# Kernel optimization log

Hardware: AMD Instinct MI355X
Metric: run time of the kernel (lower is better)

The kernel has to match this reference:

```python
import jax, jax.numpy as jnp
import numpy as np

N_NODES = 100000
N_EDGES = 300000
D_NODE_IN = 128
D_EDGE_IN = 4
LATENT = 256
HIDDEN = 256
STEPS = 6
D_OUT = 128
LN_EPS = 1e-5


def _mlp(x, w1, b1, w2, b2):
    # hk.nets.MLP([HIDDEN, out], activation=swish): act on hidden, none on output
    return jax.nn.swish(x @ w1 + b1) @ w2 + b2


def _ln(x, scale, offset):
    m = jnp.mean(x, axis=-1, keepdims=True)
    c = x - m
    v = jnp.mean(c * c, axis=-1, keepdims=True)
    return c * jax.lax.rsqrt(v + LN_EPS) * scale + offset


def setup_inputs():
    key = jax.random.key(0)
    ks = iter(jax.random.split(key, 40))

    def w(shape):
        fan_in = shape[-2]
        return (jax.random.normal(next(ks), shape, jnp.float32) / np.sqrt(fan_in).astype(np.float32))

    inp = {}
    inp['node_features'] = jax.random.normal(next(ks), (N_NODES, D_NODE_IN), jnp.float32)
    inp['edge_features'] = jax.random.normal(next(ks), (N_EDGES, D_EDGE_IN), jnp.float32)
    inp['senders'] = jax.random.randint(next(ks), (N_EDGES,), 0, N_NODES, jnp.int32)
    inp['receivers'] = jax.random.randint(next(ks), (N_EDGES,), 0, N_NODES, jnp.int32)
    # encoder (embed) MLPs + LayerNorm
    inp['enc_node_w1'] = w((D_NODE_IN, HIDDEN)); inp['enc_node_b1'] = jnp.zeros((HIDDEN,), jnp.float32)
    inp['enc_node_w2'] = w((HIDDEN, LATENT)); inp['enc_node_b2'] = jnp.zeros((LATENT,), jnp.float32)
    inp['enc_node_ln_s'] = jnp.ones((LATENT,), jnp.float32); inp['enc_node_ln_o'] = jnp.zeros((LATENT,), jnp.float32)
    inp['enc_edge_w1'] = w((D_EDGE_IN, HIDDEN)); inp['enc_edge_b1'] = jnp.zeros((HIDDEN,), jnp.float32)
    inp['enc_edge_w2'] = w((HIDDEN, LATENT)); inp['enc_edge_b2'] = jnp.zeros((LATENT,), jnp.float32)
    inp['enc_edge_ln_s'] = jnp.ones((LATENT,), jnp.float32); inp['enc_edge_ln_o'] = jnp.zeros((LATENT,), jnp.float32)
    # processor: STEPS unshared InteractionNetwork layers, weights stacked on axis 0
    inp['pe_w1'] = w((STEPS, 3 * LATENT, HIDDEN)); inp['pe_b1'] = jnp.zeros((STEPS, HIDDEN), jnp.float32)
    inp['pe_w2'] = w((STEPS, HIDDEN, LATENT)); inp['pe_b2'] = jnp.zeros((STEPS, LATENT), jnp.float32)
    inp['pe_ln_s'] = jnp.ones((STEPS, LATENT), jnp.float32); inp['pe_ln_o'] = jnp.zeros((STEPS, LATENT), jnp.float32)
    inp['pn_w1'] = w((STEPS, 2 * LATENT, HIDDEN)); inp['pn_b1'] = jnp.zeros((STEPS, HIDDEN), jnp.float32)
    inp['pn_w2'] = w((STEPS, HIDDEN, LATENT)); inp['pn_b2'] = jnp.zeros((STEPS, LATENT), jnp.float32)
    inp['pn_ln_s'] = jnp.ones((STEPS, LATENT), jnp.float32); inp['pn_ln_o'] = jnp.zeros((STEPS, LATENT), jnp.float32)
    # decoder (output) MLP, no LayerNorm
    inp['dec_w1'] = w((LATENT, HIDDEN)); inp['dec_b1'] = jnp.zeros((HIDDEN,), jnp.float32)
    inp['dec_w2'] = w((HIDDEN, D_OUT)); inp['dec_b2'] = jnp.zeros((D_OUT,), jnp.float32)
    return inp


def reference(node_features, edge_features, senders, receivers,
              enc_node_w1, enc_node_b1, enc_node_w2, enc_node_b2, enc_node_ln_s, enc_node_ln_o,
              enc_edge_w1, enc_edge_b1, enc_edge_w2, enc_edge_b2, enc_edge_ln_s, enc_edge_ln_o,
              pe_w1, pe_b1, pe_w2, pe_b2, pe_ln_s, pe_ln_o,
              pn_w1, pn_b1, pn_w2, pn_b2, pn_ln_s, pn_ln_o,
              dec_w1, dec_b1, dec_w2, dec_b2):
    # Embed nodes and edges into latent space (MLP + LayerNorm).
    node = _ln(_mlp(node_features, enc_node_w1, enc_node_b1, enc_node_w2, enc_node_b2), enc_node_ln_s, enc_node_ln_o)
    edge = _ln(_mlp(edge_features, enc_edge_w1, enc_edge_b1, enc_edge_w2, enc_edge_b2), enc_edge_ln_s, enc_edge_ln_o)

    n_nodes = node.shape[0]

    def step(carry, p):
        node, edge = carry
        ew1, eb1, ew2, eb2, els, elo, nw1, nb1, nw2, nb2, nls, nlo = p
        # edge update: MLP(concat[edge, sender_node, receiver_node]) + residual
        msg_in = jnp.concatenate([edge, node[senders], node[receivers]], axis=-1)  # [E, 3*LATENT]
        edge = edge + _ln(_mlp(msg_in, ew1, eb1, ew2, eb2), els, elo)
        # aggregate messages to receiver nodes
        agg = jax.ops.segment_sum(edge, receivers, num_segments=n_nodes)  # [N, LATENT]
        # node update: MLP(concat[node, agg]) + residual
        node = node + _ln(_mlp(jnp.concatenate([node, agg], axis=-1), nw1, nb1, nw2, nb2), nls, nlo)
        return (node, edge), None

    (node, edge), _ = jax.lax.scan(
        step, (node, edge),
        (pe_w1, pe_b1, pe_w2, pe_b2, pe_ln_s, pe_ln_o,
         pn_w1, pn_b1, pn_w2, pn_b2, pn_ln_s, pn_ln_o))

    # decoder: plain MLP (no LayerNorm) on nodes only (node_output_size given).
    return _mlp(node, dec_w1, dec_b1, dec_w2, dec_b2)  # [N, D_OUT]
```

## Files before the change

kernel.cpp:

```cpp
#include <hip/hip_runtime.h>
#include <hip/hip_bf16.h>


#define NN 100000
#define NE 300000

typedef __attribute__((ext_vector_type(8))) short bf16x8;
typedef __attribute__((ext_vector_type(8))) unsigned short u16x8;
typedef __attribute__((ext_vector_type(4))) float f32x4;

typedef const __attribute__((address_space(1))) void cg1_t;
typedef __attribute__((address_space(3))) void l3_t;
static __device__ __forceinline__ void gld_lds16(const void* g, void* l) {
  __builtin_amdgcn_global_load_lds((cg1_t*)g, (l3_t*)l, 16, 0, 0);
}

static __device__ __forceinline__ unsigned short f2bf(float f) {
  union { float f; unsigned u; } v; v.f = f;
  unsigned r = v.u + 0x7FFFu + ((v.u >> 16) & 1u);
  return (unsigned short)(r >> 16);
}
static __device__ __forceinline__ float bf2f(unsigned short h) {
  union { unsigned u; float f; } v; v.u = ((unsigned)h) << 16;
  return v.f;
}
static __device__ __forceinline__ float swish(float x) {
  return x * __builtin_amdgcn_rcpf(1.f + __expf(-x));
}

struct KArgs {
  const float* Xf;
  unsigned short* nodeB;
  unsigned short* edgeB;
  const unsigned short* aggB;
  const int* snd;
  const int* rcv;
  const unsigned short* W1p;
  const unsigned short* W2p;
  const float* b1;
  const float* b2;
  const float* lns;
  const float* lno;
  float* outF;
  int M;
};

__global__ void pack_w(const float* __restrict__ src,
                       unsigned short* __restrict__ dst,
                       int Ksrc, int Kpad, int N) {
  src += (size_t)blockIdx.y * Ksrc * N;
  dst += (size_t)blockIdx.y * Kpad * N;
  int fi = blockIdx.x;
  int nfr = N >> 4;
  int nb = fi % nfr, kb = fi / nfr;
  int t = threadIdx.x;
  int lane = t >> 3, j = t & 7;
  int k = kb * 32 + ((lane >> 4) * 8) + j;
  int col = nb * 16 + (lane & 15);
  unsigned short v = (k < Ksrc) ? f2bf(src[(size_t)k * N + col]) : (unsigned short)0;
  dst[(size_t)fi * 512 + t] = v;
}

__global__ void zero_ws(uint4* __restrict__ p, int n16) {
  uint4 z = {0u, 0u, 0u, 0u};
  for (int i = blockIdx.x * blockDim.x + threadIdx.x; i < n16;
       i += gridDim.x * blockDim.x)
    p[i] = z;
}

__global__ void hist_k(const int* __restrict__ rcv, int* __restrict__ cnt) {
  int e = blockIdx.x * blockDim.x + threadIdx.x;
  if (e < NE) {
    int r = rcv[e]; r = r < 0 ? 0 : (r > NN - 1 ? NN - 1 : r);
    atomicAdd(&cnt[r], 1);
  }
}

__global__ __launch_bounds__(1024)
void scan_k(const int* __restrict__ cnt, int* __restrict__ off) {
  __shared__ int wsum[16];
  __shared__ int carry_s, tot_s;
  int t = threadIdx.x, lane = t & 63, w = t >> 6;
  if (t == 0) carry_s = 0;
  __syncthreads();
  for (int base = 0; base < NN; base += 1024) {
    int i = base + t;
    int v = (i < NN) ? cnt[i] : 0;
    int incl = v;
    #pragma unroll
    for (int d = 1; d < 64; d <<= 1) {
      int u = __shfl_up(incl, d);
      if (lane >= d) incl += u;
    }
    if (lane == 63) wsum[w] = incl;
    int c0 = carry_s;
    __syncthreads();
    if (t < 16) {
      int s = wsum[t];
      int isc = s;
      #pragma unroll
      for (int d = 1; d < 16; d <<= 1) {
        int u = __shfl_up(isc, d);
        if (t >= d) isc += u;
      }
      wsum[t] = isc - s;
    }
    __syncthreads();
    int excl = c0 + wsum[w] + incl - v;
    if (i < NN) off[i] = excl;
    if (t == 1023) tot_s = wsum[15] + incl;
    __syncthreads();
    if (t == 0) carry_s += tot_s;
    __syncthreads();
  }
  if (t == 0) off[NN] = carry_s;
}

__global__ void fill_k(const int* __restrict__ rcv, const int* __restrict__ off,
                       int* __restrict__ cnt2, int* __restrict__ eidx) {
  int e = blockIdx.x * blockDim.x + threadIdx.x;
  if (e < NE) {
    int r = rcv[e]; r = r < 0 ? 0 : (r > NN - 1 ? NN - 1 : r);
    int p = off[r] + atomicAdd(&cnt2[r], 1);
    if (p >= 0 && p < NE) eidx[p] = e;
  }
}

__global__ __launch_bounds__(256)
void agg_k(const unsigned short* __restrict__ edge, const int* __restrict__ off,
           const int* __restrict__ eidx, unsigned short* __restrict__ agg) {
  int t = threadIdx.x;
  int n0 = blockIdx.x * 8;
  #pragma unroll 1
  for (int u = 0; u < 8; ++u) {
    int n = n0 + u;
    if (n >= NN) return;
    int s = off[n], e = off[n + 1];
    if (s < 0) s = 0;
    if (e > NE) e = NE;
    float acc = 0.f;
    for (int i = s; i < e; ++i) {
      int eid = eidx[i];
      eid = eid < 0 ? 0 : (eid > NE - 1 ? NE - 1 : eid);
      acc += bf2f(edge[(size_t)eid * 256 + t]);
    }
    agg[(size_t)n * 256 + t] = f2bf(acc);
  }
}

template<int PHASE>
__global__ __launch_bounds__(512)
void gnn_kernel(KArgs A) {
  constexpr int K1  = PHASE==0?128 : PHASE==1?64 : PHASE==2?768 : PHASE==3?512 : 256;
  constexpr int NS1 = K1 / 64;
  constexpr int N2  = (PHASE==4) ? 128 : 256;
  constexpr int NF2 = N2 / 128;

  __shared__ __align__(16) char smem[50688];
  auto Ht  = (unsigned short (*)[264])(smem + 16384);
  int*   lidx = (int*)(smem + 50176);
  float* ps    = (float*)smem;
  float* ps2   = (float*)(smem + 2048);
  float* rs_mu = (float*)(smem + 4096);
  float* rs_rs = (float*)(smem + 4352);

  const int tid  = threadIdx.x;
  const int wid  = tid >> 6;
  const int lane = tid & 63;
  const int r0   = blockIdx.x * 64;
  const int M    = A.M;

  if constexpr (PHASE == 2) {
    if (tid < 64) {
      int e = r0 + tid; if (e > M - 1) e = M - 1;
      int v = A.snd[e]; v = v < 0 ? 0 : (v > NN - 1 ? NN - 1 : v);
      lidx[tid] = v;
    } else if (tid < 128) {
      int e = r0 + tid - 64; if (e > M - 1) e = M - 1;
      int v = A.rcv[e]; v = v < 0 ? 0 : (v > NN - 1 ? NN - 1 : v);
      lidx[tid] = v;
    }
  }
  __syncthreads();

  const int mrow  = lane & 15;
  const int rbase = (lane >> 4) * 4;
  const int swz   = mrow & 7;

  f32x4 zero4 = {0.f, 0.f, 0.f, 0.f};
  f32x4 acc1[4][2];
  #pragma unroll
  for (int m = 0; m < 4; ++m) { acc1[m][0] = zero4; acc1[m][1] = zero4; }

  if constexpr (PHASE <= 1) {
    auto stage = [&](int ks, int b) {
      int r = tid >> 3;
      int c = (tid & 7) ^ (r & 7);
      int row = r0 + r; if (row > M - 1) row = M - 1;
      u16x8 w;
      if constexpr (PHASE == 0) {
        const float* s = A.Xf + (size_t)row * 128 + ks * 64 + c * 8;
        float4 f0 = *(const float4*)s;
        float4 f1 = *(const float4*)(s + 4);
        w[0]=f2bf(f0.x); w[1]=f2bf(f0.y); w[2]=f2bf(f0.z); w[3]=f2bf(f0.w);
        w[4]=f2bf(f1.x); w[5]=f2bf(f1.y); w[6]=f2bf(f1.z); w[7]=f2bf(f1.w);
      } else {
        w = (u16x8){0,0,0,0,0,0,0,0};
        if (c == 0) {
          float4 f = *(const float4*)(A.Xf + (size_t)row * 4);
          w[0]=f2bf(f.x); w[1]=f2bf(f.y); w[2]=f2bf(f.z); w[3]=f2bf(f.w);
        }
      }
      *(u16x8*)(smem + b * 8192 + (tid >> 3) * 128 + (tid & 7) * 16) = w;
    };
    stage(0, 0);
    __syncthreads();
    #pragma unroll
    for (int ks = 0; ks < NS1; ++ks) {
      if (ks + 1 < NS1) stage(ks + 1, (ks + 1) & 1);
      const char* buf = smem + (ks & 1) * 8192;
      #pragma unroll
      for (int kk = 0; kk < 2; ++kk) {
        int ch = (kk * 4 + (lane >> 4)) ^ swz;
        const char* p0 = buf + mrow * 128 + ch * 16;
        bf16x8 a0 = *(const bf16x8*)(p0);
        bf16x8 a1 = *(const bf16x8*)(p0 + 16 * 128);
        bf16x8 a2 = *(const bf16x8*)(p0 + 32 * 128);
        bf16x8 a3 = *(const bf16x8*)(p0 + 48 * 128);
        const unsigned short* wb = A.W1p + ((size_t)((2 * ks + kk) * 16 + wid * 2) * 64 + lane) * 8;
        bf16x8 b0 = *(const bf16x8*)(wb);
        bf16x8 b1 = *(const bf16x8*)(wb + 512);
        acc1[0][0] = __builtin_amdgcn_mfma_f32_16x16x32_bf16(a0, b0, acc1[0][0], 0, 0, 0);
        acc1[0][1] = __builtin_amdgcn_mfma_f32_16x16x32_bf16(a0, b1, acc1[0][1], 0, 0, 0);
        acc1[1][0] = __builtin_amdgcn_mfma_f32_16x16x32_bf16(a1, b0, acc1[1][0], 0, 0, 0);
        acc1[1][1] = __builtin_amdgcn_mfma_f32_16x16x32_bf16(a1, b1, acc1[1][1], 0, 0, 0);
        acc1[2][0] = __builtin_amdgcn_mfma_f32_16x16x32_bf16(a2, b0, acc1[2][0], 0, 0, 0);
        acc1[2][1] = __builtin_amdgcn_mfma_f32_16x16x32_bf16(a2, b1, acc1[2][1], 0, 0, 0);
        acc1[3][0] = __builtin_amdgcn_mfma_f32_16x16x32_bf16(a3, b0, acc1[3][0], 0, 0, 0);
        acc1[3][1] = __builtin_amdgcn_mfma_f32_16x16x32_bf16(a3, b1, acc1[3][1], 0, 0, 0);
      }
      __syncthreads();
    }
  } else {
    int r = tid >> 3;
    int cs = ((tid & 7) ^ (r & 7)) * 8;
    int row = r0 + r; if (row > M - 1) row = M - 1;
    const unsigned short *s0 = nullptr, *s1 = nullptr, *s2 = nullptr;
    if constexpr (PHASE == 2) {
      s0 = A.edgeB + (size_t)row * 256 + cs;
      s1 = A.nodeB + (size_t)lidx[r] * 256 + cs;
      s2 = A.nodeB + (size_t)lidx[64 + r] * 256 + cs;
    } else if constexpr (PHASE == 3) {
      s0 = A.nodeB + (size_t)row * 256 + cs;
      s1 = A.aggB + (size_t)row * 256 + cs;
    } else {
      s0 = A.nodeB + (size_t)row * 256 + cs;
    }
    auto issue = [&](int ks, int b) {
      const unsigned short* src;
      if constexpr (PHASE == 2)
        src = ks < 4 ? s0 + ks * 64 : (ks < 8 ? s1 + (ks - 4) * 64 : s2 + (ks - 8) * 64);
      else if constexpr (PHASE == 3)
        src = ks < 4 ? s0 + ks * 64 : s1 + (ks - 4) * 64;
      else
        src = s0 + ks * 64;
      gld_lds16(src, smem + b * 8192 + wid * 1024);
    };
    const unsigned short* w1base = A.W1p + ((size_t)(wid * 2) * 64 + lane) * 8;
    auto load_b = [&](int ks, bf16x8* bk0, bf16x8* bk1) {
      const unsigned short* wb0 = w1base + (size_t)(2 * ks) * 16 * 512;
      const unsigned short* wb1 = w1base + (size_t)(2 * ks + 1) * 16 * 512;
      bk0[0] = *(const bf16x8*)(wb0); bk0[1] = *(const bf16x8*)(wb0 + 512);
      bk1[0] = *(const bf16x8*)(wb1); bk1[1] = *(const bf16x8*)(wb1 + 512);
    };

    issue(0, 0);
    issue(1, 1);
    bf16x8 c0[2], c1[2], n0[2], n1[2];
    load_b(0, c0, c1);
    #pragma unroll
    for (int ks = 0; ks < NS1; ++ks) {
      if (ks < NS1 - 1) asm volatile("s_waitcnt vmcnt(1)" ::: "memory");
      else              asm volatile("s_waitcnt vmcnt(0)" ::: "memory");
      __builtin_amdgcn_sched_barrier(0);
      __builtin_amdgcn_s_barrier();
      __builtin_amdgcn_sched_barrier(0);
      if (ks + 1 < NS1) load_b(ks + 1, n0, n1);
      const char* buf = smem + (ks & 1) * 8192;
      #pragma unroll
      for (int kk = 0; kk < 2; ++kk) {
        int ch = (kk * 4 + (lane >> 4)) ^ swz;
        const char* p0 = buf + mrow * 128 + ch * 16;
        bf16x8 a0 = *(const bf16x8*)(p0);
        bf16x8 a1 = *(const bf16x8*)(p0 + 16 * 128);
        bf16x8 a2 = *(const bf16x8*)(p0 + 32 * 128);
        bf16x8 a3 = *(const bf16x8*)(p0 + 48 * 128);
        bf16x8 b0 = kk ? c1[0] : c0[0];
        bf16x8 b1 = kk ? c1[1] : c0[1];
        acc1[0][0] = __builtin_amdgcn_mfma_f32_16x16x32_bf16(a0, b0, acc1[0][0], 0, 0, 0);
        acc1[0][1] = __builtin_amdgcn_mfma_f32_16x16x32_bf16(a0, b1, acc1[0][1], 0, 0, 0);
        acc1[1][0] = __builtin_amdgcn_mfma_f32_16x16x32_bf16(a1, b0, acc1[1][0], 0, 0, 0);
        acc1[1][1] = __builtin_amdgcn_mfma_f32_16x16x32_bf16(a1, b1, acc1[1][1], 0, 0, 0);
        acc1[2][0] = __builtin_amdgcn_mfma_f32_16x16x32_bf16(a2, b0, acc1[2][0], 0, 0, 0);
        acc1[2][1] = __builtin_amdgcn_mfma_f32_16x16x32_bf16(a2, b1, acc1[2][1], 0, 0, 0);
        acc1[3][0] = __builtin_amdgcn_mfma_f32_16x16x32_bf16(a3, b0, acc1[3][0], 0, 0, 0);
        acc1[3][1] = __builtin_amdgcn_mfma_f32_16x16x32_bf16(a3, b1, acc1[3][1], 0, 0, 0);
      }
      __builtin_amdgcn_sched_barrier(0);
      __builtin_amdgcn_s_barrier();
      __builtin_amdgcn_sched_barrier(0);
      if (ks + 2 < NS1) issue(ks + 2, ks & 1);
      c0[0] = n0[0]; c0[1] = n0[1]; c1[0] = n1[0]; c1[1] = n1[1];
    }
  }

  #pragma unroll
  for (int nf = 0; nf < 2; ++nf) {
    int c = wid * 32 + nf * 16 + mrow;
    float bb = A.b1[c];
    #pragma unroll
    for (int m = 0; m < 4; ++m)
      #pragma unroll
      for (int j = 0; j < 4; ++j)
        Ht[m * 16 + rbase + j][c] = f2bf(swish(acc1[m][nf][j] + bb));
  }
  __syncthreads();

  f32x4 acc2[4][NF2];
  #pragma unroll
  for (int m = 0; m < 4; ++m)
    #pragma unroll
    for (int nf = 0; nf < NF2; ++nf) acc2[m][nf] = zero4;

  const int kof = (lane >> 4) * 8;
  #pragma unroll
  for (int ks = 0; ks < 8; ++ks) {
    bf16x8 a[4], b[NF2];
    #pragma unroll
    for (int m = 0; m < 4; ++m)
      a[m] = *(const bf16x8*)&Ht[m * 16 + mrow][ks * 32 + kof];
    #pragma unroll
    for (int nf = 0; nf < NF2; ++nf)
      b[nf] = *(const bf16x8*)(A.W2p + ((size_t)(ks * (N2 / 16) + wid * NF2 + nf) * 64 + lane) * 8);
    #pragma unroll
    for (int m = 0; m < 4; ++m)
      #pragma unroll
      for (int nf = 0; nf < NF2; ++nf)
        acc2[m][nf] = __builtin_amdgcn_mfma_f32_16x16x32_bf16(a[m], b[nf], acc2[m][nf], 0, 0, 0);
  }

  if constexpr (PHASE == 4) {
    int c = wid * 16 + mrow;
    float bb = A.b2[c];
    #pragma unroll
    for (int m = 0; m < 4; ++m)
      #pragma unroll
      for (int j = 0; j < 4; ++j) {
        int rg = r0 + m * 16 + rbase + j;
        if (rg < M) A.outF[(size_t)rg * 128 + c] = acc2[m][0][j] + bb;
      }
  } else {
    const int cc0 = wid * 32 + mrow;
    const int cc1 = cc0 + 16;
    const float bb0 = A.b2[cc0];
    const float bb1 = A.b2[cc1];
    #pragma unroll
    for (int m = 0; m < 4; ++m)
      #pragma unroll
      for (int j = 0; j < 4; ++j) {
        acc2[m][0][j] += bb0;
        acc2[m][1][j] += bb1;
        float t  = acc2[m][0][j] + acc2[m][1][j];
        float t2 = acc2[m][0][j] * acc2[m][0][j] + acc2[m][1][j] * acc2[m][1][j];
        #pragma unroll
        for (int mk = 1; mk < 16; mk <<= 1) {
          t  += __shfl_xor(t, mk);
          t2 += __shfl_xor(t2, mk);
        }
        if (mrow == 0) {
          int row = m * 16 + rbase + j;
          ps [wid * 64 + row] = t;
          ps2[wid * 64 + row] = t2;
        }
      }
    __syncthreads();
    if (tid < 64) {
      float s = 0.f, q = 0.f;
      #pragma unroll
      for (int w = 0; w < 8; ++w) { s += ps[w * 64 + tid]; q += ps2[w * 64 + tid]; }
      float mu = s * (1.0f / 256.0f);
      float va = fmaxf(q * (1.0f / 256.0f) - mu * mu, 0.f);
      rs_mu[tid] = mu;
      rs_rs[tid] = __builtin_amdgcn_rsqf(va + 1e-5f);
    }
    __syncthreads();
    const float ls0 = A.lns[cc0], lo0 = A.lno[cc0];
    const float ls1 = A.lns[cc1], lo1 = A.lno[cc1];
    #pragma unroll
    for (int m = 0; m < 4; ++m)
      #pragma unroll
      for (int j = 0; j < 4; ++j) {
        int row = m * 16 + rbase + j;
        int rg = r0 + row;
        if (rg >= M) continue;
        float mu = rs_mu[row], rstd = rs_rs[row];
        float y0 = (acc2[m][0][j] - mu) * rstd * ls0 + lo0;
        float y1 = (acc2[m][1][j] - mu) * rstd * ls1 + lo1;
        size_t base = (size_t)rg * 256;
        if constexpr (PHASE == 0) {
          A.nodeB[base + cc0] = f2bf(y0);
          A.nodeB[base + cc1] = f2bf(y1);
        } else if constexpr (PHASE == 1) {
          A.edgeB[base + cc0] = f2bf(y0);
          A.edgeB[base + cc1] = f2bf(y1);
        } else if constexpr (PHASE == 2) {
          A.edgeB[base + cc0] = f2bf(bf2f(A.edgeB[base + cc0]) + y0);
          A.edgeB[base + cc1] = f2bf(bf2f(A.edgeB[base + cc1]) + y1);
        } else {
          A.nodeB[base + cc0] = f2bf(bf2f(A.nodeB[base + cc0]) + y0);
          A.nodeB[base + cc1] = f2bf(bf2f(A.nodeB[base + cc1]) + y1);
        }
      }
  }
}

extern "C" void kernel_launch(void* const* d_in, const int* in_sizes, int n_in,
                              void* d_out, int out_size, void* d_ws, size_t ws_size,
                              hipStream_t stream) {
  (void)in_sizes; (void)n_in; (void)out_size; (void)ws_size;
  const float* x_node = (const float*)d_in[0];
  const float* x_edge = (const float*)d_in[1];
  const int* snd = (const int*)d_in[2];
  const int* rcv = (const int*)d_in[3];
  const float* en_w1 = (const float*)d_in[4];
  const float* en_b1 = (const float*)d_in[5];
  const float* en_w2 = (const float*)d_in[6];
  const float* en_b2 = (const float*)d_in[7];
  const float* en_ls = (const float*)d_in[8];
  const float* en_lo = (const float*)d_in[9];
  const float* ee_w1 = (const float*)d_in[10];
  const float* ee_b1 = (const float*)d_in[11];
  const float* ee_w2 = (const float*)d_in[12];
  const float* ee_b2 = (const float*)d_in[13];
  const float* ee_ls = (const float*)d_in[14];
  const float* ee_lo = (const float*)d_in[15];
  const float* pe_w1 = (const float*)d_in[16];
  const float* pe_b1 = (const float*)d_in[17];
  const float* pe_w2 = (const float*)d_in[18];
  const float* pe_b2 = (const float*)d_in[19];
  const float* pe_ls = (const float*)d_in[20];
  const float* pe_lo = (const float*)d_in[21];
  const float* pn_w1 = (const float*)d_in[22];
  const float* pn_b1 = (const float*)d_in[23];
  const float* pn_w2 = (const float*)d_in[24];
  const float* pn_b2 = (const float*)d_in[25];
  const float* pn_ls = (const float*)d_in[26];
  const float* pn_lo = (const float*)d_in[27];
  const float* dc_w1 = (const float*)d_in[28];
  const float* dc_b1 = (const float*)d_in[29];
  const float* dc_w2 = (const float*)d_in[30];
  const float* dc_b2 = (const float*)d_in[31];

  char* ws = (char*)d_ws;
  unsigned short* edgeB = (unsigned short*)(ws);
  unsigned short* nodeB = (unsigned short*)(ws + 153600000LL);
  unsigned short* aggB  = (unsigned short*)(ws + 204800000LL);

  unsigned short* wpck = (unsigned short*)d_out;
  size_t o = 0;
  auto nxt = [&](size_t n) { unsigned short* p = wpck + o; o += n; return p; };
  unsigned short* p_en_w1 = nxt(128 * 256);
  unsigned short* p_en_w2 = nxt(256 * 256);
  unsigned short* p_ee_w1 = nxt(64 * 256);
  unsigned short* p_ee_w2 = nxt(256 * 256);
  unsigned short* p_pe_w1 = nxt((size_t)6 * 768 * 256);
  unsigned short* p_pe_w2 = nxt((size_t)6 * 256 * 256);
  unsigned short* p_pn_w1 = nxt((size_t)6 * 512 * 256);
  unsigned short* p_pn_w2 = nxt((size_t)6 * 256 * 256);
  unsigned short* p_dc_w1 = nxt(256 * 256);
  unsigned short* p_dc_w2 = nxt(256 * 128);
  const size_t DC_BYTES = (256 * 256 + 256 * 128) * 2;

  char* outc = (char*)d_out;
  int* cnt  = (int*)(outc + 6062080);
  int* cnt2 = (int*)(outc + 6462080);
  int* off  = (int*)(outc + 6862080);
  int* eidx = (int*)(outc + 7262096);

  dim3 B(512);
  pack_w<<<dim3(4 * 16, 1), B, 0, stream>>>(en_w1, p_en_w1, 128, 128, 256);
  pack_w<<<dim3(8 * 16, 1), B, 0, stream>>>(en_w2, p_en_w2, 256, 256, 256);
  pack_w<<<dim3(2 * 16, 1), B, 0, stream>>>(ee_w1, p_ee_w1, 4, 64, 256);
  pack_w<<<dim3(8 * 16, 1), B, 0, stream>>>(ee_w2, p_ee_w2, 256, 256, 256);
  pack_w<<<dim3(24 * 16, 6), B, 0, stream>>>(pe_w1, p_pe_w1, 768, 768, 256);
  pack_w<<<dim3(8 * 16, 6), B, 0, stream>>>(pe_w2, p_pe_w2, 256, 256, 256);
  pack_w<<<dim3(16 * 16, 6), B, 0, stream>>>(pn_w1, p_pn_w1, 512, 512, 256);
  pack_w<<<dim3(8 * 16, 6), B, 0, stream>>>(pn_w2, p_pn_w2, 256, 256, 256);
  pack_w<<<dim3(8 * 16, 1), B, 0, stream>>>(dc_w1, p_dc_w1, 256, 256, 256);
  pack_w<<<dim3(8 * 8, 1), B, 0, stream>>>(dc_w2, p_dc_w2, 256, 256, 128);

  zero_ws<<<dim3(196), dim3(256), 0, stream>>>((uint4*)cnt, 800000 / 16);
  hist_k<<<dim3(1172), dim3(256), 0, stream>>>(rcv, cnt);
  scan_k<<<dim3(1), dim3(1024), 0, stream>>>(cnt, off);
  fill_k<<<dim3(1172), dim3(256), 0, stream>>>(rcv, off, cnt2, eidx);

  dim3 GN(1563), GE(4688);

  {
    KArgs a{}; a.Xf = x_node; a.W1p = p_en_w1; a.W2p = p_en_w2;
    a.b1 = en_b1; a.b2 = en_b2; a.lns = en_ls; a.lno = en_lo;
    a.nodeB = nodeB; a.M = NN;
    gnn_kernel<0><<<GN, B, 0, stream>>>(a);
  }
  {
    KArgs a{}; a.Xf = x_edge; a.W1p = p_ee_w1; a.W2p = p_ee_w2;
    a.b1 = ee_b1; a.b2 = ee_b2; a.lns = ee_ls; a.lno = ee_lo;
    a.edgeB = edgeB; a.M = NE;
    gnn_kernel<1><<<GE, B, 0, stream>>>(a);
  }
  for (int s = 0; s < 6; ++s) {
    {
      KArgs a{}; a.snd = snd; a.rcv = rcv;
      a.nodeB = nodeB; a.edgeB = edgeB;
      a.W1p = p_pe_w1 + (size_t)s * 768 * 256;
      a.W2p = p_pe_w2 + (size_t)s * 256 * 256;
      a.b1 = pe_b1 + s * 256; a.b2 = pe_b2 + s * 256;
      a.lns = pe_ls + s * 256; a.lno = pe_lo + s * 256;
      a.M = NE;
      gnn_kernel<2><<<GE, B, 0, stream>>>(a);
    }
    agg_k<<<dim3(12500), dim3(256), 0, stream>>>(edgeB, off, eidx, aggB);
    {
      KArgs a{}; a.nodeB = nodeB; a.aggB = aggB;
      a.W1p = p_pn_w1 + (size_t)s * 512 * 256;
      a.W2p = p_pn_w2 + (size_t)s * 256 * 256;
      a.b1 = pn_b1 + s * 256; a.b2 = pn_b2 + s * 256;
      a.lns = pn_ls + s * 256; a.lno = pn_lo + s * 256;
      a.M = NN;
      gnn_kernel<3><<<GN, B, 0, stream>>>(a);
    }
  }
  hipMemcpyAsync((void*)aggB, p_dc_w1, DC_BYTES, hipMemcpyDeviceToDevice, stream);
  {
    KArgs a{}; a.nodeB = nodeB;
    a.W1p = (const unsigned short*)aggB;
    a.W2p = (const unsigned short*)aggB + 256 * 256;
    a.b1 = dc_b1; a.b2 = dc_b2;
    a.outF = (float*)d_out; a.M = NN;
    gnn_kernel<4><<<GN, B, 0, stream>>>(a);
  }
}
```

Before: 2.778 ms.

## Halve block to 4 waves, each wave computing 64 output columns

The fused MLP kernel drops from 8 waves to 4 waves per 64-row tile. Each wave now owns 64 output columns (four 16-wide MFMA fragments instead of two), so every A fragment read from LDS feeds twice as many MFMAs. Staging, the LayerNorm partial-sum reduction and the epilogue are rewritten for the wider per-wave tile. The cross-iteration weight-register prefetch is replaced by loading all weight fragments after the barrier. This raises accumulator register pressure, may cut occupancy, and exposes weight-load latency.

```diff
diff --git a/kernel.cpp b/kernel.cpp
--- a/kernel.cpp
+++ b/kernel.cpp
@@ -149,20 +149,20 @@
 }
 
 template<int PHASE>
-__global__ __launch_bounds__(512)
+__global__ __launch_bounds__(256)
 void gnn_kernel(KArgs A) {
   constexpr int K1  = PHASE==0?128 : PHASE==1?64 : PHASE==2?768 : PHASE==3?512 : 256;
   constexpr int NS1 = K1 / 64;
   constexpr int N2  = (PHASE==4) ? 128 : 256;
-  constexpr int NF2 = N2 / 128;
+  constexpr int NF2 = N2 / 64;
 
   __shared__ __align__(16) char smem[50688];
   auto Ht  = (unsigned short (*)[264])(smem + 16384);
   int*   lidx = (int*)(smem + 50176);
   float* ps    = (float*)smem;
-  float* ps2   = (float*)(smem + 2048);
-  float* rs_mu = (float*)(smem + 4096);
-  float* rs_rs = (float*)(smem + 4352);
+  float* ps2   = (float*)(smem + 1024);
+  float* rs_mu = (float*)(smem + 2048);
+  float* rs_rs = (float*)(smem + 2304);
 
   const int tid  = threadIdx.x;
   const int wid  = tid >> 6;
@@ -188,30 +188,39 @@
   const int swz   = mrow & 7;
 
   f32x4 zero4 = {0.f, 0.f, 0.f, 0.f};
-  f32x4 acc1[4][2];
+  f32x4 acc1[4][4];
   #pragma unroll
-  for (int m = 0; m < 4; ++m) { acc1[m][0] = zero4; acc1[m][1] = zero4; }
+  for (int m = 0; m < 4; ++m)
+    #pragma unroll
+    for (int nf = 0; nf < 4; ++nf) acc1[m][nf] = zero4;
+
+  const int sslot = lane & 7;
+  int rj0 = wid * 16 + 0 + (lane >> 3);
+  int rj1 = wid * 16 + 8 + (lane >> 3);
 
   if constexpr (PHASE <= 1) {
     auto stage = [&](int ks, int b) {
-      int r = tid >> 3;
-      int c = (tid & 7) ^ (r & 7);
-      int row = r0 + r; if (row > M - 1) row = M - 1;
-      u16x8 w;
-      if constexpr (PHASE == 0) {
-        const float* s = A.Xf + (size_t)row * 128 + ks * 64 + c * 8;
-        float4 f0 = *(const float4*)s;
-        float4 f1 = *(const float4*)(s + 4);
-        w[0]=f2bf(f0.x); w[1]=f2bf(f0.y); w[2]=f2bf(f0.z); w[3]=f2bf(f0.w);
-        w[4]=f2bf(f1.x); w[5]=f2bf(f1.y); w[6]=f2bf(f1.z); w[7]=f2bf(f1.w);
-      } else {
-        w = (u16x8){0,0,0,0,0,0,0,0};
-        if (c == 0) {
-          float4 f = *(const float4*)(A.Xf + (size_t)row * 4);
-          w[0]=f2bf(f.x); w[1]=f2bf(f.y); w[2]=f2bf(f.z); w[3]=f2bf(f.w);
-        }
-      }
-      *(u16x8*)(smem + b * 8192 + (tid >> 3) * 128 + (tid & 7) * 16) = w;
+      #pragma unroll
+      for (int j = 0; j < 2; ++j) {
+        int r = j ? rj1 : rj0;
+        int c = sslot ^ (r & 7);
+        int row = r0 + r; if (row > M - 1) row = M - 1;
+        u16x8 w;
+        if constexpr (PHASE == 0) {
+          const float* s = A.Xf + (size_t)row * 128 + ks * 64 + c * 8;
+          float4 f0 = *(const float4*)s;
+          float4 f1 = *(const float4*)(s + 4);
+          w[0]=f2bf(f0.x); w[1]=f2bf(f0.y); w[2]=f2bf(f0.z); w[3]=f2bf(f0.w);
+          w[4]=f2bf(f1.x); w[5]=f2bf(f1.y); w[6]=f2bf(f1.z); w[7]=f2bf(f1.w);
+        } else {
+          w = (u16x8){0,0,0,0,0,0,0,0};
+          if (c == 0) {
+            float4 f = *(const float4*)(A.Xf + (size_t)row * 4);
+            w[0]=f2bf(f.x); w[1]=f2bf(f.y); w[2]=f2bf(f.z); w[3]=f2bf(f.w);
+          }
+        }
+        *(u16x8*)(smem + b * 8192 + r * 128 + sslot * 16) = w;
+      }
     };
     stage(0, 0);
     __syncthreads();
@@ -227,96 +236,94 @@
         bf16x8 a1 = *(const bf16x8*)(p0 + 16 * 128);
         bf16x8 a2 = *(const bf16x8*)(p0 + 32 * 128);
         bf16x8 a3 = *(const bf16x8*)(p0 + 48 * 128);
-        const unsigned short* wb = A.W1p + ((size_t)((2 * ks + kk) * 16 + wid * 2) * 64 + lane) * 8;
-        bf16x8 b0 = *(const bf16x8*)(wb);
-        bf16x8 b1 = *(const bf16x8*)(wb + 512);
-        acc1[0][0] = __builtin_amdgcn_mfma_f32_16x16x32_bf16(a0, b0, acc1[0][0], 0, 0, 0);
-        acc1[0][1] = __builtin_amdgcn_mfma_f32_16x16x32_bf16(a0, b1, acc1[0][1], 0, 0, 0);
-        acc1[1][0] = __builtin_amdgcn_mfma_f32_16x16x32_bf16(a1, b0, acc1[1][0], 0, 0, 0);
-        acc1[1][1] = __builtin_amdgcn_mfma_f32_16x16x32_bf16(a1, b1, acc1[1][1], 0, 0, 0);
-        acc1[2][0] = __builtin_amdgcn_mfma_f32_16x16x32_bf16(a2, b0, acc1[2][0], 0, 0, 0);
-        acc1[2][1] = __builtin_amdgcn_mfma_f32_16x16x32_bf16(a2, b1, acc1[2][1], 0, 0, 0);
-        acc1[3][0] = __builtin_amdgcn_mfma_f32_16x16x32_bf16(a3, b0, acc1[3][0], 0, 0, 0);
-        acc1[3][1] = __builtin_amdgcn_mfma_f32_16x16x32_bf16(a3, b1, acc1[3][1], 0, 0, 0);
+        #pragma unroll
+        for (int nf = 0; nf < 4; ++nf) {
+          bf16x8 b = *(const bf16x8*)(A.W1p +
+              ((size_t)((2 * ks + kk) * 16 + wid * 4 + nf) * 64 + lane) * 8);
+          acc1[0][nf] = __builtin_amdgcn_mfma_f32_16x16x32_bf16(a0, b, acc1[0][nf], 0, 0, 0);
+          acc1[1][nf] = __builtin_amdgcn_mfma_f32_16x16x32_bf16(a1, b, acc1[1][nf], 0, 0, 0);
+          acc1[2][nf] = __builtin_amdgcn_mfma_f32_16x16x32_bf16(a2, b, acc1[2][nf], 0, 0, 0);
+          acc1[3][nf] = __builtin_amdgcn_mfma_f32_16x16x32_bf16(a3, b, acc1[3][nf], 0, 0, 0);
+        }
       }
       __syncthreads();
     }
   } else {
-    int r = tid >> 3;
-    int cs = ((tid & 7) ^ (r & 7)) * 8;
-    int row = r0 + r; if (row > M - 1) row = M - 1;
-    const unsigned short *s0 = nullptr, *s1 = nullptr, *s2 = nullptr;
-    if constexpr (PHASE == 2) {
-      s0 = A.edgeB + (size_t)row * 256 + cs;
-      s1 = A.nodeB + (size_t)lidx[r] * 256 + cs;
-      s2 = A.nodeB + (size_t)lidx[64 + r] * 256 + cs;
-    } else if constexpr (PHASE == 3) {
-      s0 = A.nodeB + (size_t)row * 256 + cs;
-      s1 = A.aggB + (size_t)row * 256 + cs;
-    } else {
-      s0 = A.nodeB + (size_t)row * 256 + cs;
+    const unsigned short *p0[2], *p1[2], *p2[2];
+    #pragma unroll
+    for (int j = 0; j < 2; ++j) {
+      int r = j ? rj1 : rj0;
+      int cs = (sslot ^ (r & 7)) * 8;
+      int row = r0 + r; if (row > M - 1) row = M - 1;
+      if constexpr (PHASE == 2) {
+        p0[j] = A.edgeB + (size_t)row * 256 + cs;
+        p1[j] = A.nodeB + (size_t)lidx[r] * 256 + cs;
+        p2[j] = A.nodeB + (size_t)lidx[64 + r] * 256 + cs;
+      } else if constexpr (PHASE == 3) {
+        p0[j] = A.nodeB + (size_t)row * 256 + cs;
+        p1[j] = A.aggB + (size_t)row * 256 + cs;
+      } else {
+        p0[j] = A.nodeB + (size_t)row * 256 + cs;
+      }
     }
     auto issue = [&](int ks, int b) {
-      const unsigned short* src;
-      if constexpr (PHASE == 2)
-        src = ks < 4 ? s0 + ks * 64 : (ks < 8 ? s1 + (ks - 4) * 64 : s2 + (ks - 8) * 64);
-      else if constexpr (PHASE == 3)
-        src = ks < 4 ? s0 + ks * 64 : s1 + (ks - 4) * 64;
-      else
-        src = s0 + ks * 64;
-      gld_lds16(src, smem + b * 8192 + wid * 1024);
-    };
-    const unsigned short* w1base = A.W1p + ((size_t)(wid * 2) * 64 + lane) * 8;
-    auto load_b = [&](int ks, bf16x8* bk0, bf16x8* bk1) {
-      const unsigned short* wb0 = w1base + (size_t)(2 * ks) * 16 * 512;
-      const unsigned short* wb1 = w1base + (size_t)(2 * ks + 1) * 16 * 512;
-      bk0[0] = *(const bf16x8*)(wb0); bk0[1] = *(const bf16x8*)(wb0 + 512);
-      bk1[0] = *(const bf16x8*)(wb1); bk1[1] = *(const bf16x8*)(wb1 + 512);
+      #pragma unroll
+      for (int j = 0; j < 2; ++j) {
+        const unsigned short* src;
+        if constexpr (PHASE == 2)
+          src = ks < 4 ? p0[j] + ks * 64
+              : (ks < 8 ? p1[j] + (ks - 4) * 64 : p2[j] + (ks - 8) * 64);
+        else if constexpr (PHASE == 3)
+          src = ks < 4 ? p0[j] + ks * 64 : p1[j] + (ks - 4) * 64;
+        else
+          src = p0[j] + ks * 64;
+        gld_lds16(src, smem + b * 8192 + wid * 2048 + j * 1024);
+      }
     };
 
     issue(0, 0);
     issue(1, 1);
-    bf16x8 c0[2], c1[2], n0[2], n1[2];
-    load_b(0, c0, c1);
     #pragma unroll
     for (int ks = 0; ks < NS1; ++ks) {
-      if (ks < NS1 - 1) asm volatile("s_waitcnt vmcnt(1)" ::: "memory");
+      if (ks < NS1 - 1) asm volatile("s_waitcnt vmcnt(2)" ::: "memory");
       else              asm volatile("s_waitcnt vmcnt(0)" ::: "memory");
       __builtin_amdgcn_sched_barrier(0);
       __builtin_amdgcn_s_barrier();
       __builtin_amdgcn_sched_barrier(0);
-      if (ks + 1 < NS1) load_b(ks + 1, n0, n1);
       const char* buf = smem + (ks & 1) * 8192;
+      bf16x8 bw[2][4];
+      #pragma unroll
+      for (int kk = 0; kk < 2; ++kk)
+        #pragma unroll
+        for (int nf = 0; nf < 4; ++nf)
+          bw[kk][nf] = *(const bf16x8*)(A.W1p +
+              ((size_t)((2 * ks + kk) * 16 + wid * 4 + nf) * 64 + lane) * 8);
       #pragma unroll
       for (int kk = 0; kk < 2; ++kk) {
         int ch = (kk * 4 + (lane >> 4)) ^ swz;
-        const char* p0 = buf + mrow * 128 + ch * 16;
-        bf16x8 a0 = *(const bf16x8*)(p0);
-        bf16x8 a1 = *(const bf16x8*)(p0 + 16 * 128);
-        bf16x8 a2 = *(const bf16x8*)(p0 + 32 * 128);
-        bf16x8 a3 = *(const bf16x8*)(p0 + 48 * 128);
-        bf16x8 b0 = kk ? c1[0] : c0[0];
-        bf16x8 b1 = kk ? c1[1] : c0[1];
-        acc1[0][0] = __builtin_amdgcn_mfma_f32_16x16x32_bf16(a0, b0, acc1[0][0], 0, 0, 0);
-        acc1[0][1] = __builtin_amdgcn_mfma_f32_16x16x32_bf16(a0, b1, acc1[0][1], 0, 0, 0);
-        acc1[1][0] = __builtin_amdgcn_mfma_f32_16x16x32_bf16(a1, b0, acc1[1][0], 0, 0, 0);
-        acc1[1][1] = __builtin_amdgcn_mfma_f32_16x16x32_bf16(a1, b1, acc1[1][1], 0, 0, 0);
-        acc1[2][0] = __builtin_amdgcn_mfma_f32_16x16x32_bf16(a2, b0, acc1[2][0], 0, 0, 0);
-        acc1[2][1] = __builtin_amdgcn_mfma_f32_16x16x32_bf16(a2, b1, acc1[2][1], 0, 0, 0);
-        acc1[3][0] = __builtin_amdgcn_mfma_f32_16x16x32_bf16(a3, b0, acc1[3][0], 0, 0, 0);
-        acc1[3][1] = __builtin_amdgcn_mfma_f32_16x16x32_bf16(a3, b1, acc1[3][1], 0, 0, 0);
+        const char* p = buf + mrow * 128 + ch * 16;
+        bf16x8 a0 = *(const bf16x8*)(p);
+        bf16x8 a1 = *(const bf16x8*)(p + 16 * 128);
+        bf16x8 a2 = *(const bf16x8*)(p + 32 * 128);
+        bf16x8 a3 = *(const bf16x8*)(p + 48 * 128);
+        #pragma unroll
+        for (int nf = 0; nf < 4; ++nf) {
+          acc1[0][nf] = __builtin_amdgcn_mfma_f32_16x16x32_bf16(a0, bw[kk][nf], acc1[0][nf], 0, 0, 0);
+          acc1[1][nf] = __builtin_amdgcn_mfma_f32_16x16x32_bf16(a1, bw[kk][nf], acc1[1][nf], 0, 0, 0);
+          acc1[2][nf] = __builtin_amdgcn_mfma_f32_16x16x32_bf16(a2, bw[kk][nf], acc1[2][nf], 0, 0, 0);
+          acc1[3][nf] = __builtin_amdgcn_mfma_f32_16x16x32_bf16(a3, bw[kk][nf], acc1[3][nf], 0, 0, 0);
+        }
       }
       __builtin_amdgcn_sched_barrier(0);
       __builtin_amdgcn_s_barrier();
       __builtin_amdgcn_sched_barrier(0);
       if (ks + 2 < NS1) issue(ks + 2, ks & 1);
-      c0[0] = n0[0]; c0[1] = n0[1]; c1[0] = n1[0]; c1[1] = n1[1];
     }
   }
 
   #pragma unroll
-  for (int nf = 0; nf < 2; ++nf) {
-    int c = wid * 32 + nf * 16 + mrow;
+  for (int nf = 0; nf < 4; ++nf) {
+    int c = wid * 64 + nf * 16 + mrow;
     float bb = A.b1[c];
     #pragma unroll
     for (int m = 0; m < 4; ++m)
@@ -350,28 +357,39 @@
   }
 
   if constexpr (PHASE == 4) {
-    int c = wid * 16 + mrow;
-    float bb = A.b2[c];
+    #pragma unroll
+    for (int nf = 0; nf < NF2; ++nf) {
+      int c = wid * 32 + nf * 16 + mrow;
+      float bb = A.b2[c];
+      #pragma unroll
+      for (int m = 0; m < 4; ++m)
+        #pragma unroll
+        for (int j = 0; j < 4; ++j) {
+          int rg = r0 + m * 16 + rbase + j;
+          if (rg < M) A.outF[(size_t)rg * 128 + c] = acc2[m][nf][j] + bb;
+        }
+    }
+  } else {
+    float bb[4], ls[4], lo[4];
+    int cc[4];
+    #pragma unroll
+    for (int nf = 0; nf < 4; ++nf) {
+      cc[nf] = wid * 64 + nf * 16 + mrow;
+      bb[nf] = A.b2[cc[nf]];
+      ls[nf] = A.lns[cc[nf]];
+      lo[nf] = A.lno[cc[nf]];
+    }
     #pragma unroll
     for (int m = 0; m < 4; ++m)
       #pragma unroll
       for (int j = 0; j < 4; ++j) {
-        int rg = r0 + m * 16 + rbase + j;
-        if (rg < M) A.outF[(size_t)rg * 128 + c] = acc2[m][0][j] + bb;
-      }
-  } else {
-    const int cc0 = wid * 32 + mrow;
-    const int cc1 = cc0 + 16;
-    const float bb0 = A.b2[cc0];
-    const float bb1 = A.b2[cc1];
-    #pragma unroll
-    for (int m = 0; m < 4; ++m)
-      #pragma unroll
-      for (int j = 0; j < 4; ++j) {
-        acc2[m][0][j] += bb0;
-        acc2[m][1][j] += bb1;
-        float t  = acc2[m][0][j] + acc2[m][1][j];
-        float t2 = acc2[m][0][j] * acc2[m][0][j] + acc2[m][1][j] * acc2[m][1][j];
+        float t = 0.f, t2 = 0.f;
+        #pragma unroll
+        for (int nf = 0; nf < 4; ++nf) {
+          acc2[m][nf][j] += bb[nf];
+          t  += acc2[m][nf][j];
+          t2 += acc2[m][nf][j] * acc2[m][nf][j];
+        }
         #pragma unroll
         for (int mk = 1; mk < 16; mk <<= 1) {
           t  += __shfl_xor(t, mk);
@@ -387,15 +405,13 @@
     if (tid < 64) {
       float s = 0.f, q = 0.f;
       #pragma unroll
-      for (int w = 0; w < 8; ++w) { s += ps[w * 64 + tid]; q += ps2[w * 64 + tid]; }
+      for (int w = 0; w < 4; ++w) { s += ps[w * 64 + tid]; q += ps2[w * 64 + tid]; }
       float mu = s * (1.0f / 256.0f);
       float va = fmaxf(q * (1.0f / 256.0f) - mu * mu, 0.f);
       rs_mu[tid] = mu;
       rs_rs[tid] = __builtin_amdgcn_rsqf(va + 1e-5f);
     }
     __syncthreads();
-    const float ls0 = A.lns[cc0], lo0 = A.lno[cc0];
-    const float ls1 = A.lns[cc1], lo1 = A.lno[cc1];
     #pragma unroll
     for (int m = 0; m < 4; ++m)
       #pragma unroll
@@ -404,21 +420,19 @@
         int rg = r0 + row;
         if (rg >= M) continue;
         float mu = rs_mu[row], rstd = rs_rs[row];
-        float y0 = (acc2[m][0][j] - mu) * rstd * ls0 + lo0;
-        float y1 = (acc2[m][1][j] - mu) * rstd * ls1 + lo1;
         size_t base = (size_t)rg * 256;
-        if constexpr (PHASE == 0) {
-          A.nodeB[base + cc0] = f2bf(y0);
-          A.nodeB[base + cc1] = f2bf(y1);
-        } else if constexpr (PHASE == 1) {
-          A.edgeB[base + cc0] = f2bf(y0);
-          A.edgeB[base + cc1] = f2bf(y1);
-        } else if constexpr (PHASE == 2) {
-          A.edgeB[base + cc0] = f2bf(bf2f(A.edgeB[base + cc0]) + y0);
-          A.edgeB[base + cc1] = f2bf(bf2f(A.edgeB[base + cc1]) + y1);
-        } else {
-          A.nodeB[base + cc0] = f2bf(bf2f(A.nodeB[base + cc0]) + y0);
-          A.nodeB[base + cc1] = f2bf(bf2f(A.nodeB[base + cc1]) + y1);
+        #pragma unroll
+        for (int nf = 0; nf < 4; ++nf) {
+          float y = (acc2[m][nf][j] - mu) * rstd * ls[nf] + lo[nf];
+          if constexpr (PHASE == 0) {
+            A.nodeB[base + cc[nf]] = f2bf(y);
+          } else if constexpr (PHASE == 1) {
+            A.edgeB[base + cc[nf]] = f2bf(y);
+          } else if constexpr (PHASE == 2) {
+            A.edgeB[base + cc[nf]] = f2bf(bf2f(A.edgeB[base + cc[nf]]) + y);
+          } else {
+            A.nodeB[base + cc[nf]] = f2bf(bf2f(A.nodeB[base + cc[nf]]) + y);
+          }
         }
       }
   }
@@ -487,7 +501,7 @@
   int* off  = (int*)(outc + 6862080);
   int* eidx = (int*)(outc + 7262096);
 
-  dim3 B(512);
+  dim3 B(512), BG(256);
   pack_w<<<dim3(4 * 16, 1), B, 0, stream>>>(en_w1, p_en_w1, 128, 128, 256);
   pack_w<<<dim3(8 * 16, 1), B, 0, stream>>>(en_w2, p_en_w2, 256, 256, 256);
   pack_w<<<dim3(2 * 16, 1), B, 0, stream>>>(ee_w1, p_ee_w1, 4, 64, 256);
@@ -510,13 +524,13 @@
     KArgs a{}; a.Xf = x_node; a.W1p = p_en_w1; a.W2p = p_en_w2;
     a.b1 = en_b1; a.b2 = en_b2; a.lns = en_ls; a.lno = en_lo;
     a.nodeB = nodeB; a.M = NN;
-    gnn_kernel<0><<<GN, B, 0, stream>>>(a);
+    gnn_kernel<0><<<GN, BG, 0, stream>>>(a);
   }
   {
     KArgs a{}; a.Xf = x_edge; a.W1p = p_ee_w1; a.W2p = p_ee_w2;
     a.b1 = ee_b1; a.b2 = ee_b2; a.lns = ee_ls; a.lno = ee_lo;
     a.edgeB = edgeB; a.M = NE;
-    gnn_kernel<1><<<GE, B, 0, stream>>>(a);
+    gnn_kernel<1><<<GE, BG, 0, stream>>>(a);
   }
   for (int s = 0; s < 6; ++s) {
     {
@@ -527,7 +541,7 @@
       a.b1 = pe_b1 + s * 256; a.b2 = pe_b2 + s * 256;
       a.lns = pe_ls + s * 256; a.lno = pe_lo + s * 256;
       a.M = NE;
-      gnn_kernel<2><<<GE, B, 0, stream>>>(a);
+      gnn_kernel<2><<<GE, BG, 0, stream>>>(a);
     }
     agg_k<<<dim3(12500), dim3(256), 0, stream>>>(edgeB, off, eidx, aggB);
     {
@@ -537,7 +551,7 @@
       a.b1 = pn_b1 + s * 256; a.b2 = pn_b2 + s * 256;
       a.lns = pn_ls + s * 256; a.lno = pn_lo + s * 256;
       a.M = NN;
-      gnn_kernel<3><<<GN, B, 0, stream>>>(a);
+      gnn_kernel<3><<<GN, BG, 0, stream>>>(a);
     }
   }
   hipMemcpyAsync((void*)aggB, p_dc_w1, DC_BYTES, hipMemcpyDeviceToDevice, stream);
@@ -547,6 +561,6 @@
     a.W2p = (const unsigned short*)aggB + 256 * 256;
     a.b1 = dc_b1; a.b2 = dc_b2;
     a.outF = (float*)d_out; a.M = NN;
-    gnn_kernel<4><<<GN, B, 0, stream>>>(a);
-  }
-}
+    gnn_kernel<4><<<GN, BG, 0, stream>>>(a);
+  }
+}
```

Measured after the change: 3.555 ms. 28.0% more time.
